# Performance work log

Hardware: AMD Instinct MI355X
Metric: run time of the kernel (lower is better)

## Reference

```python
import jax, jax.numpy as jnp
from jax import lax
import numpy as np

N = 262144
D_IN = 32
D_HID = 128
N_HIDDEN = 8          # total hidden Linear+ReLU layers (first + 7 repeated)
D_OUT = 16
D_COND_IN = 16
D_COND_OUT = 3


def setup_inputs() -> dict:
    key = jax.random.key(0)
    ks = jax.random.split(key, 8)
    s = 0.05  # stand-in for kaiming-uniform scale; math shape-faithful
    x = jax.random.normal(ks[0], (N, D_IN), dtype=jnp.float32)
    cond = jax.random.normal(ks[1], (N, D_COND_IN), dtype=jnp.float32)
    W0 = jax.random.normal(ks[2], (D_HID, D_IN), dtype=jnp.float32) * s
    Wh = jax.random.normal(ks[3], (N_HIDDEN - 1, D_HID, D_HID), dtype=jnp.float32) * s
    Wout = jax.random.normal(ks[4], (D_OUT, D_HID), dtype=jnp.float32) * s
    Wc0 = jax.random.normal(ks[5], (D_HID, D_HID + D_COND_IN), dtype=jnp.float32) * s
    Wc1 = jax.random.normal(ks[6], (D_HID // 2, D_HID), dtype=jnp.float32) * s
    Wc2 = jax.random.normal(ks[7], (D_COND_OUT, D_HID // 2), dtype=jnp.float32) * s
    return {"x": x, "cond": cond, "W0": W0, "Wh": Wh, "Wout": Wout,
            "Wc0": Wc0, "Wc1": Wc1, "Wc2": Wc2}


def reference(x, cond, W0, Wh, Wout, Wc0, Wc1, Wc2):
    # backbone: Linear(no bias) -> ReLU, repeated
    h = jax.nn.relu(x @ W0.T)                       # [N, D_HID]

    def step(h, W):
        return jax.nn.relu(h @ W.T), None

    h, _ = lax.scan(step, h, Wh)                    # 7 more Linear+ReLU layers

    uncond_x = h @ Wout.T                           # [N, D_OUT], no activation

    # conditional sub-net: Linear (NO activation) -> Linear -> ReLU -> Linear
    z = jnp.concatenate([h, cond], axis=-1) @ Wc0.T  # [N, D_HID]
    z = jax.nn.relu(z @ Wc1.T)                       # [N, D_HID//2]
    cond_x = z @ Wc2.T                               # [N, D_COND_OUT]
    return (uncond_x, cond_x)
```

## Files before the change

kernel.cpp:

```cpp
#include <hip/hip_runtime.h>
#include <hip/hip_bf16.h>
#include <stdint.h>


typedef __attribute__((ext_vector_type(8)))  short short8;
typedef __attribute__((ext_vector_type(16))) float f32x16;
typedef __attribute__((ext_vector_type(4)))  float float4v;

#define NTOT 262144

#define CW0    0
#define CWH(i) (8192 + (i) * 32768)
#define CWOUT  237568
#define CWC0   245760
#define CWC1   278528
#define CWC2   294912
#define WS_TOTAL 299008

__device__ __forceinline__ unsigned short f2bf(float v) {
  union { __hip_bfloat16 h; unsigned short u; } c;
  c.h = __float2bfloat16(v);
  return c.u;
}

__global__ __launch_bounds__(256) void convw(
    const float* __restrict__ W0, const float* __restrict__ Wh,
    const float* __restrict__ Wout, const float* __restrict__ Wc0,
    const float* __restrict__ Wc1, const float* __restrict__ Wc2,
    unsigned char* __restrict__ ws) {
  int cid = blockIdx.x * 256 + threadIdx.x;
  if (cid >= WS_TOTAL / 16) return;
  int b = cid * 16;
  const float* src; int base, rows, SS, NKT;
  if (b < 8192)        { base = CW0;   src = W0;   rows = 128; SS = 32;  NKT = 2; }
  else if (b < 237568) { int i = (b - 8192) >> 15;
                         base = 8192 + (i << 15);
                         src = Wh + i * 16384;      rows = 128; SS = 128; NKT = 8; }
  else if (b < 245760) { base = CWOUT; src = Wout; rows = 16;  SS = 128; NKT = 8; }
  else if (b < 278528) { base = CWC0;  src = Wc0;  rows = 128; SS = 144; NKT = 8; }
  else if (b < 294912) { base = CWC1;  src = Wc1;  rows = 64;  SS = 128; NKT = 8; }
  else                 { base = CWC2;  src = Wc2;  rows = 3;   SS = 64;  NKT = 4; }
  int rel = b - base;
  int c   = rel >> 10;
  int t   = c / NKT, kk = c - t * NKT;
  int l   = (rel & 1023) >> 4;
  int n   = l & 31, g = l >> 5;
  int row = 32 * t + n, col = 16 * kk + 8 * g;
  unsigned w0 = 0, w1 = 0, w2 = 0, w3 = 0;
  if (row < rows) {
    const float* p = src + row * SS + col;
    w0 = (unsigned)f2bf(p[0]) | ((unsigned)f2bf(p[1]) << 16);
    w1 = (unsigned)f2bf(p[2]) | ((unsigned)f2bf(p[3]) << 16);
    w2 = (unsigned)f2bf(p[4]) | ((unsigned)f2bf(p[5]) << 16);
    w3 = (unsigned)f2bf(p[6]) | ((unsigned)f2bf(p[7]) << 16);
  }
  *(uint4*)(ws + b) = make_uint4(w0, w1, w2, w3);
}

__device__ __forceinline__ unsigned pk2(float a, float b) {
  unsigned d;
  asm("v_cvt_pk_bf16_f32 %0, %1, %2" : "=v"(d) : "v"(a), "v"(b));
  return d;
}

__device__ __forceinline__ short8 frag_s8(const unsigned (&f)[4]) {
  union { unsigned u[4]; short8 s; } c;
  c.u[0] = f[0]; c.u[1] = f[1]; c.u[2] = f[2]; c.u[3] = f[3];
  return c.s;
}

__device__ __forceinline__ void swap32(unsigned &a, unsigned &b) {
  asm("v_permlane32_swap_b32 %0, %1" : "+v"(a), "+v"(b));
}

__device__ __forceinline__ void build2(const f32x16 &a,
                                       unsigned (&f0)[4], unsigned (&f1)[4]) {
  unsigned a00 = pk2(a[0], a[1]),   a01 = pk2(a[2], a[3]);
  unsigned b00 = pk2(a[4], a[5]),   b01 = pk2(a[6], a[7]);
  swap32(a00, b00); swap32(a01, b01);
  f0[0] = a00; f0[1] = a01; f0[2] = b00; f0[3] = b01;
  unsigned a10 = pk2(a[8],  a[9]),  a11 = pk2(a[10], a[11]);
  unsigned b10 = pk2(a[12], a[13]), b11 = pk2(a[14], a[15]);
  swap32(a10, b10); swap32(a11, b11);
  f1[0] = a10; f1[1] = a11; f1[2] = b10; f1[3] = b11;
}

__device__ __forceinline__ void stage(const unsigned char* __restrict__ g,
                                      unsigned char* l, int bytes,
                                      int wv, int lane) {
  #pragma unroll
  for (int base = wv * 1024; base < bytes; base += 4096) {
    __builtin_amdgcn_global_load_lds(
        (const __attribute__((address_space(1))) void*)(g + base + lane * 16),
        (__attribute__((address_space(3))) void*)(l + base), 16, 0, 0);
  }
}

#define VMCNT_(N) asm volatile("s_waitcnt vmcnt(" #N ")" ::: "memory")
#define VMCNT(N) VMCNT_(N)
#define BAR() __builtin_amdgcn_s_barrier()
#define SETPRIO(x) __builtin_amdgcn_s_setprio(x)
#define MFMA(A_, B_, C_) __builtin_amdgcn_mfma_f32_32x32x16_bf16(A_, B_, C_, 0, 0, 0)

template <int NKT, bool RELU>
__device__ __forceinline__ void half_phase(const unsigned char* lb,
                                           const unsigned (&cur)[2][8][4],
                                           unsigned (&nxt)[2][8][4], int hb,
                                           const f32x16 &zero16) {
  f32x16 a[2][2];
  SETPRIO(1);
  #pragma unroll
  for (int kk = 0; kk < NKT; ++kk) {
    short8 wf0 = *(const short8*)(lb + kk * 1024);
    short8 wf1 = *(const short8*)(lb + NKT * 1024 + kk * 1024);
    if (kk == 0) {
      a[0][0] = MFMA(wf0, frag_s8(cur[0][0]), zero16);
      a[0][1] = MFMA(wf0, frag_s8(cur[1][0]), zero16);
      a[1][0] = MFMA(wf1, frag_s8(cur[0][0]), zero16);
      a[1][1] = MFMA(wf1, frag_s8(cur[1][0]), zero16);
    } else {
      a[0][0] = MFMA(wf0, frag_s8(cur[0][kk]), a[0][0]);
      a[0][1] = MFMA(wf0, frag_s8(cur[1][kk]), a[0][1]);
      a[1][0] = MFMA(wf1, frag_s8(cur[0][kk]), a[1][0]);
      a[1][1] = MFMA(wf1, frag_s8(cur[1][kk]), a[1][1]);
    }
  }
  SETPRIO(0);
  #pragma unroll
  for (int u = 0; u < 2; ++u)
    #pragma unroll
    for (int s = 0; s < 2; ++s) {
      if (RELU) {
        #pragma unroll
        for (int j = 0; j < 16; ++j) a[u][s][j] = fmaxf(a[u][s][j], 0.f);
      }
      build2(a[u][s], nxt[s][hb + 2 * u], nxt[s][hb + 2 * u + 1]);
    }
}

__device__ __forceinline__ void half_c9(const unsigned char* lb,
                                        const unsigned (&cur)[2][8][4],
                                        unsigned (&nxt)[2][8][4], int hb,
                                        const unsigned (&cw0)[4],
                                        const unsigned (&cw1)[4],
                                        const unsigned (&cf)[2][4],
                                        const f32x16 &zero16) {
  f32x16 a[2][2];
  SETPRIO(1);
  #pragma unroll
  for (int kk = 0; kk < 8; ++kk) {
    short8 wf0 = *(const short8*)(lb + kk * 1024);
    short8 wf1 = *(const short8*)(lb + 8192 + kk * 1024);
    if (kk == 0) {
      a[0][0] = MFMA(wf0, frag_s8(cur[0][0]), zero16);
      a[0][1] = MFMA(wf0, frag_s8(cur[1][0]), zero16);
      a[1][0] = MFMA(wf1, frag_s8(cur[0][0]), zero16);
      a[1][1] = MFMA(wf1, frag_s8(cur[1][0]), zero16);
    } else {
      a[0][0] = MFMA(wf0, frag_s8(cur[0][kk]), a[0][0]);
      a[0][1] = MFMA(wf0, frag_s8(cur[1][kk]), a[0][1]);
      a[1][0] = MFMA(wf1, frag_s8(cur[0][kk]), a[1][0]);
      a[1][1] = MFMA(wf1, frag_s8(cur[1][kk]), a[1][1]);
    }
  }
  a[0][0] = MFMA(frag_s8(cw0), frag_s8(cf[0]), a[0][0]);
  a[0][1] = MFMA(frag_s8(cw0), frag_s8(cf[1]), a[0][1]);
  a[1][0] = MFMA(frag_s8(cw1), frag_s8(cf[0]), a[1][0]);
  a[1][1] = MFMA(frag_s8(cw1), frag_s8(cf[1]), a[1][1]);
  SETPRIO(0);
  #pragma unroll
  for (int u = 0; u < 2; ++u)
    #pragma unroll
    for (int s = 0; s < 2; ++s)
      build2(a[u][s], nxt[s][hb + 2 * u], nxt[s][hb + 2 * u + 1]);
}

__global__ __launch_bounds__(256, 2) void mlp_fused(
    const float* __restrict__ x, const float* __restrict__ cond,
    const float* __restrict__ wc0g, const unsigned char* __restrict__ ws,
    float* __restrict__ out) {
  __shared__ __align__(16) unsigned char lds[49152];

  const int tid  = threadIdx.x;
  const int lane = tid & 63;
  const int wv   = tid >> 6;
  const int g    = lane >> 5;
  const int n    = lane & 31;
  const int rowbase = blockIdx.x * 256 + wv * 64;
  const int r0 = rowbase + n;
  const int r1 = rowbase + 32 + n;
  const unsigned char* ldsL = lds + lane * 16;

  f32x16 zero16;
  #pragma unroll
  for (int j = 0; j < 16; ++j) zero16[j] = 0.f;

  unsigned FA[2][8][4], FB[2][8][4];

  #pragma unroll
  for (int s = 0; s < 2; ++s) {
    int row = s ? r1 : r0;
    #pragma unroll
    for (int kk = 0; kk < 2; ++kk) {
      const float4v* p = (const float4v*)(x + row * 32 + kk * 16 + 8 * g);
      float4v u0 = p[0], u1 = p[1];
      FA[s][kk][0] = pk2(u0.x, u0.y);
      FA[s][kk][1] = pk2(u0.z, u0.w);
      FA[s][kk][2] = pk2(u1.x, u1.y);
      FA[s][kk][3] = pk2(u1.z, u1.w);
    }
  }
  stage(ws + CW0,        lds,         4096, wv, lane);
  stage(ws + CW0 + 4096, lds + 16384, 4096, wv, lane);
  VMCNT(1); BAR();

  stage(ws + CWH(0),         lds + 32768, 16384, wv, lane);
  half_phase<2, true>(ldsL,          FA, FB, 0, zero16);
  VMCNT(4); BAR();
  stage(ws + CWH(0) + 16384, lds,         16384, wv, lane);
  half_phase<2, true>(ldsL + 16384,  FA, FB, 4, zero16);
  VMCNT(4); BAR();

  stage(ws + CWH(1),         lds + 16384, 16384, wv, lane);
  half_phase<8, true>(ldsL + 32768,  FB, FA, 0, zero16);
  VMCNT(4); BAR();
  stage(ws + CWH(1) + 16384, lds + 32768, 16384, wv, lane);
  half_phase<8, true>(ldsL,          FB, FA, 4, zero16);
  VMCNT(4); BAR();

  stage(ws + CWH(2),         lds,         16384, wv, lane);
  half_phase<8, true>(ldsL + 16384,  FA, FB, 0, zero16);
  VMCNT(4); BAR();
  stage(ws + CWH(2) + 16384, lds + 16384, 16384, wv, lane);
  half_phase<8, true>(ldsL + 32768,  FA, FB, 4, zero16);
  VMCNT(4); BAR();

  stage(ws + CWH(3),         lds + 32768, 16384, wv, lane);
  half_phase<8, true>(ldsL,          FB, FA, 0, zero16);
  VMCNT(4); BAR();
  stage(ws + CWH(3) + 16384, lds,         16384, wv, lane);
  half_phase<8, true>(ldsL + 16384,  FB, FA, 4, zero16);
  VMCNT(4); BAR();

  stage(ws + CWH(4),         lds + 16384, 16384, wv, lane);
  half_phase<8, true>(ldsL + 32768,  FA, FB, 0, zero16);
  VMCNT(4); BAR();
  stage(ws + CWH(4) + 16384, lds + 32768, 16384, wv, lane);
  half_phase<8, true>(ldsL,          FA, FB, 4, zero16);
  VMCNT(4); BAR();

  stage(ws + CWH(5),         lds,         16384, wv, lane);
  half_phase<8, true>(ldsL + 16384,  FB, FA, 0, zero16);
  VMCNT(4); BAR();
  stage(ws + CWH(5) + 16384, lds + 16384, 16384, wv, lane);
  half_phase<8, true>(ldsL + 32768,  FB, FA, 4, zero16);
  VMCNT(4); BAR();

  stage(ws + CWH(6),         lds + 32768, 16384, wv, lane);
  half_phase<8, true>(ldsL,          FA, FB, 0, zero16);
  VMCNT(4); BAR();
  stage(ws + CWH(6) + 16384, lds,         16384, wv, lane);
  half_phase<8, true>(ldsL + 16384,  FA, FB, 4, zero16);
  VMCNT(4); BAR();

  stage(ws + CWOUT, lds + 16384, 8192, wv, lane);
  half_phase<8, true>(ldsL + 32768,  FB, FA, 0, zero16);
  VMCNT(2); BAR();
  stage(ws + CWC0, lds + 32768, 16384, wv, lane);
  half_phase<8, true>(ldsL,          FB, FA, 4, zero16);
  VMCNT(4); BAR();

  unsigned CF[2][4];
  {
    stage(ws + CWC0 + 16384, lds, 16384, wv, lane);
    #pragma unroll
    for (int s = 0; s < 2; ++s) {
      const float4v* q = (const float4v*)(cond + (s ? r1 : r0) * 16 + 8 * g);
      float4v c0 = q[0], c1 = q[1];
      CF[s][0] = pk2(c0.x, c0.y); CF[s][1] = pk2(c0.z, c0.w);
      CF[s][2] = pk2(c1.x, c1.y); CF[s][3] = pk2(c1.z, c1.w);
    }
    const unsigned char* lb = ldsL + 16384;
    f32x16 a0, a1;
    SETPRIO(1);
    #pragma unroll
    for (int kk = 0; kk < 8; ++kk) {
      short8 wf = *(const short8*)(lb + kk * 1024);
      if (kk == 0) {
        a0 = MFMA(wf, frag_s8(FA[0][0]), zero16);
        a1 = MFMA(wf, frag_s8(FA[1][0]), zero16);
      } else {
        a0 = MFMA(wf, frag_s8(FA[0][kk]), a0);
        a1 = MFMA(wf, frag_s8(FA[1][kk]), a1);
      }
    }
    SETPRIO(0);
    *(float4v*)(out + r0 * 16 + 4 * g)     = (float4v){a0[0], a0[1], a0[2], a0[3]};
    *(float4v*)(out + r0 * 16 + 8 + 4 * g) = (float4v){a0[4], a0[5], a0[6], a0[7]};
    *(float4v*)(out + r1 * 16 + 4 * g)     = (float4v){a1[0], a1[1], a1[2], a1[3]};
    *(float4v*)(out + r1 * 16 + 8 + 4 * g) = (float4v){a1[4], a1[5], a1[6], a1[7]};
  }
  VMCNT(12); BAR();

  {
    unsigned CW0r[4], CW1r[4];
    #pragma unroll
    for (int u = 0; u < 2; ++u) {
      const float4v* pc = (const float4v*)(wc0g + (32 * u + n) * 144 + 128 + 8 * g);
      float4v q0 = pc[0], q1 = pc[1];
      unsigned* cw = u ? CW1r : CW0r;
      cw[0] = pk2(q0.x, q0.y); cw[1] = pk2(q0.z, q0.w);
      cw[2] = pk2(q1.x, q1.y); cw[3] = pk2(q1.z, q1.w);
    }
    stage(ws + CWC1, lds, 16384, wv, lane);
    half_c9(ldsL + 32768, FA, FB, 0, CW0r, CW1r, CF, zero16);
  }
  VMCNT(16); BAR();

  {
    unsigned CW0r[4], CW1r[4];
    #pragma unroll
    for (int u = 0; u < 2; ++u) {
      const float4v* pc = (const float4v*)(wc0g + (32 * (2 + u) + n) * 144 + 128 + 8 * g);
      float4v q0 = pc[0], q1 = pc[1];
      unsigned* cw = u ? CW1r : CW0r;
      cw[0] = pk2(q0.x, q0.y); cw[1] = pk2(q0.z, q0.w);
      cw[2] = pk2(q1.x, q1.y); cw[3] = pk2(q1.z, q1.w);
    }
    stage(ws + CWC2, lds + 16384, 4096, wv, lane);
    half_c9(ldsL, FA, FB, 4, CW0r, CW1r, CF, zero16);
  }
  VMCNT(5); BAR();

  half_phase<8, true>(ldsL, FB, FA, 0, zero16);
  VMCNT(0); BAR();

  {
    const unsigned char* lb = ldsL + 16384;
    f32x16 a0, a1;
    #pragma unroll
    for (int kk = 0; kk < 4; ++kk) {
      short8 wf = *(const short8*)(lb + kk * 1024);
      if (kk == 0) {
        a0 = MFMA(wf, frag_s8(FA[0][0]), zero16);
        a1 = MFMA(wf, frag_s8(FA[1][0]), zero16);
      } else {
        a0 = MFMA(wf, frag_s8(FA[0][kk]), a0);
        a1 = MFMA(wf, frag_s8(FA[1][kk]), a1);
      }
    }
    float* outc = out + (size_t)NTOT * 16;
    if (g == 0) {
      outc[r0 * 3 + 0] = a0[0];
      outc[r0 * 3 + 1] = a0[1];
      outc[r0 * 3 + 2] = a0[2];
      outc[r1 * 3 + 0] = a1[0];
      outc[r1 * 3 + 1] = a1[1];
      outc[r1 * 3 + 2] = a1[2];
    }
  }
}

extern "C" void kernel_launch(void* const* d_in, const int* in_sizes, int n_in,
                              void* d_out, int out_size, void* d_ws, size_t ws_size,
                              hipStream_t stream) {
  const float* x    = (const float*)d_in[0];
  const float* cond = (const float*)d_in[1];
  const float* W0   = (const float*)d_in[2];
  const float* Wh   = (const float*)d_in[3];
  const float* Wout = (const float*)d_in[4];
  const float* Wc0  = (const float*)d_in[5];
  const float* Wc1  = (const float*)d_in[6];
  const float* Wc2  = (const float*)d_in[7];
  unsigned char* ws = (unsigned char*)d_ws;

  convw<<<dim3((WS_TOTAL / 16 + 255) / 256), dim3(256), 0, stream>>>(
      W0, Wh, Wout, Wc0, Wc1, Wc2, ws);
  mlp_fused<<<dim3(NTOT / 256), dim3(256), 0, stream>>>(
      x, cond, Wc0, ws, (float*)d_out);
}
```

Baseline: 79.43 us.

## Shrink weight staging from triple to double LDS buffering with full waits

Reduces the shared-memory weight ring from three 16KB slots to two, alternating between two buffers, and replaces the partial vmcnt waits with full drains before each barrier. The smaller LDS footprint could let more blocks reside per CU or cut LDS pressure. In exchange, each stage's global load gets only one phase of overlap instead of two, and the full waits may expose load latency.

```diff
diff --git a/kernel.cpp b/kernel.cpp
--- a/kernel.cpp
+++ b/kernel.cpp
@@ -179,7 +179,7 @@
     const float* __restrict__ x, const float* __restrict__ cond,
     const float* __restrict__ wc0g, const unsigned char* __restrict__ ws,
     float* __restrict__ out) {
-  __shared__ __align__(16) unsigned char lds[49152];
+  __shared__ __align__(16) unsigned char lds[32768];
 
   const int tid  = threadIdx.x;
   const int lane = tid & 63;
@@ -189,7 +189,8 @@
   const int rowbase = blockIdx.x * 256 + wv * 64;
   const int r0 = rowbase + n;
   const int r1 = rowbase + 32 + n;
-  const unsigned char* ldsL = lds + lane * 16;
+  const unsigned char* B0 = lds + lane * 16;
+  const unsigned char* B1 = B0 + 16384;
 
   f32x16 zero16;
   #pragma unroll
@@ -197,6 +198,7 @@
 
   unsigned FA[2][8][4], FB[2][8][4];
 
+  stage(ws + CW0, lds, 8192, wv, lane);
   #pragma unroll
   for (int s = 0; s < 2; ++s) {
     int row = s ? r1 : r0;
@@ -210,69 +212,65 @@
       FA[s][kk][3] = pk2(u1.z, u1.w);
     }
   }
-  stage(ws + CW0,        lds,         4096, wv, lane);
-  stage(ws + CW0 + 4096, lds + 16384, 4096, wv, lane);
-  VMCNT(1); BAR();
-
-  stage(ws + CWH(0),         lds + 32768, 16384, wv, lane);
-  half_phase<2, true>(ldsL,          FA, FB, 0, zero16);
-  VMCNT(4); BAR();
-  stage(ws + CWH(0) + 16384, lds,         16384, wv, lane);
-  half_phase<2, true>(ldsL + 16384,  FA, FB, 4, zero16);
-  VMCNT(4); BAR();
-
-  stage(ws + CWH(1),         lds + 16384, 16384, wv, lane);
-  half_phase<8, true>(ldsL + 32768,  FB, FA, 0, zero16);
-  VMCNT(4); BAR();
-  stage(ws + CWH(1) + 16384, lds + 32768, 16384, wv, lane);
-  half_phase<8, true>(ldsL,          FB, FA, 4, zero16);
-  VMCNT(4); BAR();
-
-  stage(ws + CWH(2),         lds,         16384, wv, lane);
-  half_phase<8, true>(ldsL + 16384,  FA, FB, 0, zero16);
-  VMCNT(4); BAR();
-  stage(ws + CWH(2) + 16384, lds + 16384, 16384, wv, lane);
-  half_phase<8, true>(ldsL + 32768,  FA, FB, 4, zero16);
-  VMCNT(4); BAR();
-
-  stage(ws + CWH(3),         lds + 32768, 16384, wv, lane);
-  half_phase<8, true>(ldsL,          FB, FA, 0, zero16);
-  VMCNT(4); BAR();
-  stage(ws + CWH(3) + 16384, lds,         16384, wv, lane);
-  half_phase<8, true>(ldsL + 16384,  FB, FA, 4, zero16);
-  VMCNT(4); BAR();
-
-  stage(ws + CWH(4),         lds + 16384, 16384, wv, lane);
-  half_phase<8, true>(ldsL + 32768,  FA, FB, 0, zero16);
-  VMCNT(4); BAR();
-  stage(ws + CWH(4) + 16384, lds + 32768, 16384, wv, lane);
-  half_phase<8, true>(ldsL,          FA, FB, 4, zero16);
-  VMCNT(4); BAR();
-
-  stage(ws + CWH(5),         lds,         16384, wv, lane);
-  half_phase<8, true>(ldsL + 16384,  FB, FA, 0, zero16);
-  VMCNT(4); BAR();
-  stage(ws + CWH(5) + 16384, lds + 16384, 16384, wv, lane);
-  half_phase<8, true>(ldsL + 32768,  FB, FA, 4, zero16);
-  VMCNT(4); BAR();
-
-  stage(ws + CWH(6),         lds + 32768, 16384, wv, lane);
-  half_phase<8, true>(ldsL,          FA, FB, 0, zero16);
-  VMCNT(4); BAR();
-  stage(ws + CWH(6) + 16384, lds,         16384, wv, lane);
-  half_phase<8, true>(ldsL + 16384,  FA, FB, 4, zero16);
-  VMCNT(4); BAR();
-
+  VMCNT(0); BAR();
+
+  stage(ws + CWH(0), lds + 16384, 16384, wv, lane);
+  half_phase<2, true>(B0,        FA, FB, 0, zero16);
+  half_phase<2, true>(B0 + 4096, FA, FB, 4, zero16);
+  VMCNT(0); BAR();
+
+  stage(ws + CWH(0) + 16384, lds, 16384, wv, lane);
+  half_phase<8, true>(B1, FB, FA, 0, zero16);
+  VMCNT(0); BAR();
+  stage(ws + CWH(1), lds + 16384, 16384, wv, lane);
+  half_phase<8, true>(B0, FB, FA, 4, zero16);
+  VMCNT(0); BAR();
+
+  stage(ws + CWH(1) + 16384, lds, 16384, wv, lane);
+  half_phase<8, true>(B1, FA, FB, 0, zero16);
+  VMCNT(0); BAR();
+  stage(ws + CWH(2), lds + 16384, 16384, wv, lane);
+  half_phase<8, true>(B0, FA, FB, 4, zero16);
+  VMCNT(0); BAR();
+
+  stage(ws + CWH(2) + 16384, lds, 16384, wv, lane);
+  half_phase<8, true>(B1, FB, FA, 0, zero16);
+  VMCNT(0); BAR();
+  stage(ws + CWH(3), lds + 16384, 16384, wv, lane);
+  half_phase<8, true>(B0, FB, FA, 4, zero16);
+  VMCNT(0); BAR();
+
+  stage(ws + CWH(3) + 16384, lds, 16384, wv, lane);
+  half_phase<8, true>(B1, FA, FB, 0, zero16);
+  VMCNT(0); BAR();
+  stage(ws + CWH(4), lds + 16384, 16384, wv, lane);
+  half_phase<8, true>(B0, FA, FB, 4, zero16);
+  VMCNT(0); BAR();
+
+  stage(ws + CWH(4) + 16384, lds, 16384, wv, lane);
+  half_phase<8, true>(B1, FB, FA, 0, zero16);
+  VMCNT(0); BAR();
+  stage(ws + CWH(5), lds + 16384, 16384, wv, lane);
+  half_phase<8, true>(B0, FB, FA, 4, zero16);
+  VMCNT(0); BAR();
+
+  stage(ws + CWH(5) + 16384, lds, 16384, wv, lane);
+  half_phase<8, true>(B1, FA, FB, 0, zero16);
+  VMCNT(0); BAR();
+  stage(ws + CWH(6), lds + 16384, 16384, wv, lane);
+  half_phase<8, true>(B0, FA, FB, 4, zero16);
+  VMCNT(0); BAR();
+
+  stage(ws + CWH(6) + 16384, lds, 16384, wv, lane);
+  half_phase<8, true>(B1, FB, FA, 0, zero16);
+  VMCNT(0); BAR();
   stage(ws + CWOUT, lds + 16384, 8192, wv, lane);
-  half_phase<8, true>(ldsL + 32768,  FB, FA, 0, zero16);
-  VMCNT(2); BAR();
-  stage(ws + CWC0, lds + 32768, 16384, wv, lane);
-  half_phase<8, true>(ldsL,          FB, FA, 4, zero16);
-  VMCNT(4); BAR();
+  half_phase<8, true>(B0, FB, FA, 4, zero16);
+  VMCNT(0); BAR();
 
   unsigned CF[2][4];
   {
-    stage(ws + CWC0 + 16384, lds, 16384, wv, lane);
+    stage(ws + CWC0, lds, 16384, wv, lane);
     #pragma unroll
     for (int s = 0; s < 2; ++s) {
       const float4v* q = (const float4v*)(cond + (s ? r1 : r0) * 16 + 8 * g);
@@ -280,12 +278,11 @@
       CF[s][0] = pk2(c0.x, c0.y); CF[s][1] = pk2(c0.z, c0.w);
       CF[s][2] = pk2(c1.x, c1.y); CF[s][3] = pk2(c1.z, c1.w);
     }
-    const unsigned char* lb = ldsL + 16384;
     f32x16 a0, a1;
     SETPRIO(1);
     #pragma unroll
     for (int kk = 0; kk < 8; ++kk) {
-      short8 wf = *(const short8*)(lb + kk * 1024);
+      short8 wf = *(const short8*)(B1 + kk * 1024);
       if (kk == 0) {
         a0 = MFMA(wf, frag_s8(FA[0][0]), zero16);
         a1 = MFMA(wf, frag_s8(FA[1][0]), zero16);
@@ -300,9 +297,10 @@
     *(float4v*)(out + r1 * 16 + 4 * g)     = (float4v){a1[0], a1[1], a1[2], a1[3]};
     *(float4v*)(out + r1 * 16 + 8 + 4 * g) = (float4v){a1[4], a1[5], a1[6], a1[7]};
   }
-  VMCNT(12); BAR();
+  VMCNT(0); BAR();
 
   {
+    stage(ws + CWC0 + 16384, lds + 16384, 16384, wv, lane);
     unsigned CW0r[4], CW1r[4];
     #pragma unroll
     for (int u = 0; u < 2; ++u) {
@@ -312,12 +310,12 @@
       cw[0] = pk2(q0.x, q0.y); cw[1] = pk2(q0.z, q0.w);
       cw[2] = pk2(q1.x, q1.y); cw[3] = pk2(q1.z, q1.w);
     }
+    half_c9(B0, FA, FB, 0, CW0r, CW1r, CF, zero16);
+  }
+  VMCNT(0); BAR();
+
+  {
     stage(ws + CWC1, lds, 16384, wv, lane);
-    half_c9(ldsL + 32768, FA, FB, 0, CW0r, CW1r, CF, zero16);
-  }
-  VMCNT(16); BAR();
-
-  {
     unsigned CW0r[4], CW1r[4];
     #pragma unroll
     for (int u = 0; u < 2; ++u) {
@@ -327,20 +325,19 @@
       cw[0] = pk2(q0.x, q0.y); cw[1] = pk2(q0.z, q0.w);
       cw[2] = pk2(q1.x, q1.y); cw[3] = pk2(q1.z, q1.w);
     }
-    stage(ws + CWC2, lds + 16384, 4096, wv, lane);
-    half_c9(ldsL, FA, FB, 4, CW0r, CW1r, CF, zero16);
-  }
-  VMCNT(5); BAR();
-
-  half_phase<8, true>(ldsL, FB, FA, 0, zero16);
+    half_c9(B1, FA, FB, 4, CW0r, CW1r, CF, zero16);
+  }
+  VMCNT(0); BAR();
+
+  stage(ws + CWC2, lds + 16384, 4096, wv, lane);
+  half_phase<8, true>(B0, FB, FA, 0, zero16);
   VMCNT(0); BAR();
 
   {
-    const unsigned char* lb = ldsL + 16384;
     f32x16 a0, a1;
     #pragma unroll
     for (int kk = 0; kk < 4; ++kk) {
-      short8 wf = *(const short8*)(lb + kk * 1024);
+      short8 wf = *(const short8*)(B1 + kk * 1024);
       if (kk == 0) {
         a0 = MFMA(wf, frag_s8(FA[0][0]), zero16);
         a1 = MFMA(wf, frag_s8(FA[1][0]), zero16);
```

Measured after the change: 80.79 us. Within noise of the previous version (+1.7%).
